# Kernel tuning notes

Hardware: AMD Instinct MI355X
Metric: run time of the kernel (lower is better)

The kernel has to match this reference:

```python
import math
import jax, jax.numpy as jnp
import numpy as np

# ---- module hyperparameters (from init_kwargs) ----
MAX_DISP = 48
IMG_WIDTH = 1248
W = IMG_WIDTH // 4          # 312 rows of the OT problem (left pixels)
C_COLS = MAX_DISP + W       # 360 columns (shifted right pixels)
NUM_ITER = 10
TAU = 0.95
EPS = 1.0
KAPPA = (1.0 - TAU) / 2.0
XI = (1.0 - TAU) / (1.0 + TAU)
RHO = EPS * TAU / (1.0 - TAU)
BIG_COST = 10000.0

B, H = 2, 64


def setup_inputs() -> dict:
    key = jax.random.key(0)
    scores = jax.random.normal(key, (B, MAX_DISP, H, W), dtype=jnp.float32)
    return {"scores": scores}


def _masked(x):
    # torch.where(isfinite(x), x, 0)
    return jnp.where(jnp.isfinite(x), x, jnp.zeros_like(x))


def _lse_kernel(Cm, f, g, axis):
    # S = (C - f[...,None] - g[...,None,:]) / eps ; eps*logsumexp(-S, axis)
    S = (Cm - f[..., None] - g[..., None, :]) / EPS
    w_res = EPS * jax.nn.logsumexp(-S, axis=axis)
    w_sgn = f if axis == -1 else g
    return w_res - _masked(w_sgn)


def _sinkhorn_update(Cm, f, g, axis, log_marginal):
    app = _lse_kernel(Cm, f, g, axis)
    return EPS * log_marginal - _masked(app)


def _smin(h, log_marginal):
    return -RHO * jax.nn.logsumexp(-h / RHO + log_marginal, axis=-1)


def _unbalanced_ot(Cm):
    # Cm: (B,H,W,C_COLS) cost matrix
    log_a = jnp.full((W,), -math.log(W), dtype=Cm.dtype)
    log_b = jnp.full((C_COLS,), -math.log(C_COLS), dtype=Cm.dtype)

    f = -EPS * jax.nn.logsumexp(-Cm / EPS + log_b, axis=-1)          # (B,H,W)
    g = jnp.zeros(Cm.shape[:2] + (C_COLS,), dtype=Cm.dtype)          # (B,H,C)

    for _ in range(NUM_ITER):
        old_f = f
        new_g = TAU * _sinkhorn_update(Cm, old_f, g, axis=-2, log_marginal=log_b)
        new_g = new_g - KAPPA * _smin(old_f, log_a)[..., None]
        new_g = new_g + XI * _smin(new_g, log_b)[..., None]
        new_f = TAU * _sinkhorn_update(Cm, f, new_g, axis=-1, log_marginal=log_a)
        new_f = new_f - KAPPA * _smin(new_g, log_b)[..., None]
        new_f = new_f + XI * _smin(new_f, log_a)[..., None]
        f, g = new_f, new_g

    S = (Cm - f[..., None] - g[..., None, :]) / EPS
    return jnp.exp(-S)                                               # transport plan P


def _scatter_to_cost(scores):
    # (B,D,H,W) scores -> (B,H,W,C_COLS) cost, vectorized scatter over d
    Bn, D, Hn, Wn = scores.shape
    j = jnp.arange(Wn)
    d = jnp.arange(D)
    col = j[None, :] - d[:, None] + MAX_DISP                          # (D,W), all in-range, no collisions
    jj = jnp.broadcast_to(j[None, :], (D, Wn))
    cost = jnp.full((Bn, Hn, Wn, C_COLS), BIG_COST, dtype=scores.dtype)
    # scores (B,D,H,W) -> (B,H,D,W) to match fancy-index result shape
    cost = cost.at[:, :, jj, col].set(-jnp.transpose(scores, (0, 2, 1, 3)))
    return cost


def _plan_to_disparity(P, D):
    right = jnp.arange(C_COLS, dtype=P.dtype) - D
    left = jnp.arange(W, dtype=P.dtype)
    disp_map = left[:, None] - right[None, :]                         # (W,C)
    mass = jnp.clip(jnp.sum(P, axis=-1), 1e-8, None)                  # (B,H,W)
    disp = jnp.sum(P * disp_map, axis=-1) / mass                      # (B,H,W)
    return disp[:, None, :, :]                                        # (B,1,H,W)


def reference(scores):
    D = scores.shape[1]
    Cm = _scatter_to_cost(scores)
    P = _unbalanced_ot(Cm)
    return _plan_to_disparity(P, D)
```

## Files before the change

kernel.cpp:

```cpp
#include <hip/hip_runtime.h>
#include <math.h>


#define MAXD   48
#define WROWS  312
#define CCOLS  360
#define NITER  10
#define NT     768
#define NWAVE  12
#define KD     24
#define NACC   (2 * NITER + 1)

__device__ __forceinline__ float pair_sum(float x) {
    int y = __builtin_amdgcn_update_dpp(0, __float_as_int(x), 0xB1, 0xf, 0xf, true);
    return x + __int_as_float(y);
}
template <int CTRL>
__device__ __forceinline__ float dpp_add(float x, float acc) {
    int y = __builtin_amdgcn_update_dpp(0, __float_as_int(x), CTRL, 0xf, 0xf, true);
    return acc + __int_as_float(y);
}
__device__ __forceinline__ float dpp_sum64(float x) {
    x = dpp_add<0x111>(x, x);
    x = dpp_add<0x112>(x, x);
    x = dpp_add<0x114>(x, x);
    x = dpp_add<0x118>(x, x);
    x = dpp_add<0x142>(x, x);
    x = dpp_add<0x143>(x, x);
    return x;
}

__global__ __launch_bounds__(NT, 3)
void ot_disp_kernel(const float* __restrict__ scores, float* __restrict__ out) {
    const int bid  = blockIdx.x;
    const int tid  = threadIdx.x;
    const int half = tid >> 1;
    const int sub  = tid & 1;
    const int wid  = tid >> 6;

    const float LOG_A2 = -8.2854022f;
    const float LOG_B2 = -8.4918531f;
    const float TAU    = 0.95f;
    const float KAPPA  = 0.025f;
    const float XI     = 0.025641026f;
    const float RHO    = 19.0f;
    const float INVRHO = 0.052631579f;
    const float TIR    = 0.05f;

    __shared__ float2 sEA[204], sEB[205], sGA[180], sGB[181];
    __shared__ __align__(16) float s_lg[NACC][384];
    __shared__ float s_R[NACC];
    float* const EAf = (float*)sEA;  float* const EBf = (float*)sEB;
    float* const GAf = (float*)sGA;  float* const GBf = (float*)sGB;

    {
        float4* lg4 = (float4*)&s_lg[0][0];
        #pragma unroll
        for (int i = 0; i < 3; ++i) {
            int idx = tid + i * NT;
            if (idx < NACC * 96) lg4[idx] = make_float4(-1e30f, -1e30f, -1e30f, -1e30f);
        }
    }
    if (tid < 205) {
        sEB[tid] = make_float2(0.f, 0.f);
        if (tid < 204) sEA[tid] = make_float2(0.f, 0.f);
        if (tid < 181) sGB[tid] = make_float2(0.f, 0.f);
        if (tid < 180) sGA[tid] = make_float2(0.f, 0.f);
    }

    const bool rowAct = (half < WROWS);
    const bool colAct = (half >= 1 && half < CCOLS);
    const int b = bid >> 6, h = bid & 63;
    const float* src = scores + ((size_t)(b * MAXD) * 64 + h) * WROWS;
    const size_t dstr = (size_t)64 * WROWS;
    const int d0 = sub * KD;
    const int jr = rowAct ? half : 0;
    const int jc = colAct ? half : 0;

    float wcol[KD];
    float wrowR[KD];
    #pragma unroll
    for (int m = 0; m < KD; ++m) {
        wrowR[m] = __expf(src[dstr * (size_t)(d0 + 23 - m) + jr]);
        int j = jc - MAXD + d0 + m;
        bool v = colAct && ((unsigned)j < (unsigned)WROWS);
        float sv = src[dstr * (size_t)(d0 + m) + (v ? j : 0)];
        wcol[m] = v ? __expf(sv) : 0.0f;
    }

    const int pe = jc + d0;
    const float2* const ep = (pe & 1) ? (sEB + ((pe + 1) >> 1)) : (sEA + (pe >> 1));
    const int qg = jr + 25 - d0;
    const float2* const gp = (qg & 1) ? (sGB + ((qg + 1) >> 1)) : (sGA + (qg >> 1));

    __syncthreads();

    {
        float a0=0,a1=0,a2=0,a3=0;
        #pragma unroll
        for (int m = 0; m < KD; m += 4) {
            a0 += wrowR[m];   a1 += wrowR[m+1];
            a2 += wrowR[m+2]; a3 += wrowR[m+3];
        }
        float s  = pair_sum((a0 + a1) + (a2 + a3));
        float ls = __builtin_amdgcn_logf(s);
        float eh = __builtin_amdgcn_exp2f(-ls);
        if (rowAct && sub == 0) {
            EAf[half + MAXD] = eh; EBf[half + MAXD + 1] = eh;
            s_lg[0][half] = ls;
        }
        __syncthreads();
    }

    float2 gv[12];
    float ehat = 0.f, den = 0.f;
    for (int it = 0; it < NITER; ++it) {
        float a0=0,a1=0,a2=0,a3=0;
        #pragma unroll
        for (int u = 0; u < 12; u += 2) {
            float2 v0 = ep[u], v1 = ep[u+1];
            a0 = fmaf(wcol[2*u],   v0.x, a0);
            a1 = fmaf(wcol[2*u+1], v0.y, a1);
            a2 = fmaf(wcol[2*u+2], v1.x, a2);
            a3 = fmaf(wcol[2*u+3], v1.y, a3);
        }
        float cs  = pair_sum((a0 + a1) + (a2 + a3));
        float lcs = __builtin_amdgcn_logf(cs);
        float gh  = __builtin_amdgcn_exp2f(-TAU * lcs);
        if (colAct && sub == 0) {
            GAf[half] = gh; GBf[half + 1] = gh;
            s_lg[1 + 2*it][half] = lcs;
        }
        __syncthreads();

        float b0=0,b1=0,b2=0,b3=0;
        #pragma unroll
        for (int u = 0; u < 12; u += 2) {
            gv[u] = gp[u]; gv[u+1] = gp[u+1];
            b0 = fmaf(wrowR[2*u],   gv[u].x,   b0);
            b1 = fmaf(wrowR[2*u+1], gv[u].y,   b1);
            b2 = fmaf(wrowR[2*u+2], gv[u+1].x, b2);
            b3 = fmaf(wrowR[2*u+3], gv[u+1].y, b3);
        }
        den = pair_sum((b0 + b1) + (b2 + b3));
        float lrs = __builtin_amdgcn_logf(den);
        ehat = __builtin_amdgcn_exp2f(-TAU * lrs);
        if (rowAct && sub == 0) {
            EAf[half + MAXD] = ehat; EBf[half + MAXD + 1] = ehat;
            s_lg[2 + 2*it][half] = lrs;
        }
        __syncthreads();
    }

    {
        const int lane = tid & 63;
        for (int t = wid; t < NACC; t += NWAVE) {
            const float coef = (t == 0) ? INVRHO : TIR;
            const float cst  = (t & 1)  ? LOG_B2 : LOG_A2;
            float s = 0.f;
            #pragma unroll
            for (int k = 0; k < 6; ++k)
                s += __builtin_amdgcn_exp2f(fmaf(coef, s_lg[t][lane + 64*k], cst));
            s = dpp_sum64(s);
            if (lane == 63) s_R[t] = __builtin_amdgcn_logf(s);
        }
        __syncthreads();
    }

    float fsh   = -LOG_B2;
    float sminF = fsh - RHO * s_R[0];
    float gsh   = 0.f;
    #pragma unroll
    for (int it = 0; it < NITER; ++it) {
        float Cg = TAU * (LOG_B2 - fsh) - KAPPA * sminF;
        float sg = Cg - RHO * s_R[1 + 2*it];
        gsh = Cg + XI * sg;
        float sminG = (1.0f + XI) * sg;
        float Cf = TAU * (LOG_A2 - gsh) - KAPPA * sminG;
        float sf = Cf - RHO * s_R[2 + 2*it];
        fsh   = Cf + XI * sf;
        sminF = (1.0f + XI) * sf;
    }

    float n0 = 0.f, n1 = 0.f;
    #pragma unroll
    for (int u = 0; u < 12; ++u) {
        n0 = fmaf((float)(d0 + 23 - 2*u) * wrowR[2*u],   gv[u].x, n0);
        n1 = fmaf((float)(d0 + 22 - 2*u) * wrowR[2*u+1], gv[u].y, n1);
    }
    float num = pair_sum(n0 + n1);
    if (rowAct && sub == 0) {
        float E = __builtin_amdgcn_exp2f(fsh + gsh) * ehat;
        float mass = fmaxf(E * den, 1e-8f);
        out[(size_t)bid * WROWS + half] = (E * num) / mass;
    }
}

extern "C" void kernel_launch(void* const* d_in, const int* in_sizes, int n_in,
                              void* d_out, int out_size, void* d_ws, size_t ws_size,
                              hipStream_t stream) {
    const float* scores = (const float*)d_in[0];
    float* out = (float*)d_out;
    ot_disp_kernel<<<128, NT, 0, stream>>>(scores, out);
}
```

Baseline: 24.56 us.

## Store Sinkhorn kernel weights and scaling vectors in fp16 and use fdot2

Converts the per-thread exp-score weights and the shared E/G scaling vectors from fp32 to fp16. The inner products now use packed v_dot2 fp16 instructions with fp32 accumulation. The shared vectors are stored as four shifted copies so each thread can do aligned 8-byte half4 loads regardless of its start offset. This halves register use for the weights and the LDS traffic per iteration. The cost is reduced precision: fp16 weights exp(score) can overflow for large scores and lose accuracy, and the scaling factors may underflow.

```diff
diff --git a/kernel.cpp b/kernel.cpp
--- a/kernel.cpp
+++ b/kernel.cpp
@@ -1,6 +1,10 @@
 #include <hip/hip_runtime.h>
 #include <math.h>
 
+
+typedef _Float16 half1;
+typedef _Float16 half2v __attribute__((ext_vector_type(2)));
+typedef _Float16 half4v __attribute__((ext_vector_type(4)));
 
 #define MAXD   48
 #define WROWS  312
@@ -10,6 +14,8 @@
 #define NWAVE  12
 #define KD     24
 #define NACC   (2 * NITER + 1)
+#define ESTR   412
+#define GSTR   364
 
 __device__ __forceinline__ float pair_sum(float x) {
     int y = __builtin_amdgcn_update_dpp(0, __float_as_int(x), 0xB1, 0xf, 0xf, true);
@@ -47,12 +53,17 @@
     const float INVRHO = 0.052631579f;
     const float TIR    = 0.05f;
 
-    __shared__ float2 sEA[204], sEB[205], sGA[180], sGB[181];
+    __shared__ __align__(8) half1 sE[4 * ESTR];
+    __shared__ __align__(8) half1 sG[4 * GSTR];
     __shared__ __align__(16) float s_lg[NACC][384];
     __shared__ float s_R[NACC];
-    float* const EAf = (float*)sEA;  float* const EBf = (float*)sEB;
-    float* const GAf = (float*)sGA;  float* const GBf = (float*)sGB;
-
+
+    {
+        unsigned* z = (unsigned*)sE;
+        for (int i = tid; i < 824; i += NT) z[i] = 0u;
+        unsigned* zg = (unsigned*)sG;
+        for (int i = tid; i < 728; i += NT) zg[i] = 0u;
+    }
     {
         float4* lg4 = (float4*)&s_lg[0][0];
         #pragma unroll
@@ -60,12 +71,6 @@
             int idx = tid + i * NT;
             if (idx < NACC * 96) lg4[idx] = make_float4(-1e30f, -1e30f, -1e30f, -1e30f);
         }
-    }
-    if (tid < 205) {
-        sEB[tid] = make_float2(0.f, 0.f);
-        if (tid < 204) sEA[tid] = make_float2(0.f, 0.f);
-        if (tid < 181) sGB[tid] = make_float2(0.f, 0.f);
-        if (tid < 180) sGA[tid] = make_float2(0.f, 0.f);
     }
 
     const bool rowAct = (half < WROWS);
@@ -77,76 +82,84 @@
     const int jr = rowAct ? half : 0;
     const int jc = colAct ? half : 0;
 
-    float wcol[KD];
-    float wrowR[KD];
+    half2v wcolH[12];
+    half2v wrowH[12];
+    float swr = 0.0f;
     #pragma unroll
     for (int m = 0; m < KD; ++m) {
-        wrowR[m] = __expf(src[dstr * (size_t)(d0 + 23 - m) + jr]);
+        float wr = __expf(src[dstr * (size_t)(d0 + 23 - m) + jr]);
+        swr += wr;
+        wrowH[m >> 1][m & 1] = (half1)wr;
         int j = jc - MAXD + d0 + m;
         bool v = colAct && ((unsigned)j < (unsigned)WROWS);
-        float sv = src[dstr * (size_t)(d0 + m) + (v ? j : 0)];
-        wcol[m] = v ? __expf(sv) : 0.0f;
+        float wc = v ? __expf(src[dstr * (size_t)(d0 + m) + (v ? j : 0)]) : 0.0f;
+        wcolH[m >> 1][m & 1] = (half1)wc;
     }
 
     const int pe = jc + d0;
-    const float2* const ep = (pe & 1) ? (sEB + ((pe + 1) >> 1)) : (sEA + (pe >> 1));
+    const int rE = (4 - (pe & 3)) & 3;
+    const half4v* const epk = (const half4v*)(sE + rE * ESTR + pe + rE);
     const int qg = jr + 25 - d0;
-    const float2* const gp = (qg & 1) ? (sGB + ((qg + 1) >> 1)) : (sGA + (qg >> 1));
+    const int rG = (4 - (qg & 3)) & 3;
+    const half4v* const gpk = (const half4v*)(sG + rG * GSTR + qg + rG);
 
     __syncthreads();
 
     {
-        float a0=0,a1=0,a2=0,a3=0;
-        #pragma unroll
-        for (int m = 0; m < KD; m += 4) {
-            a0 += wrowR[m];   a1 += wrowR[m+1];
-            a2 += wrowR[m+2]; a3 += wrowR[m+3];
-        }
-        float s  = pair_sum((a0 + a1) + (a2 + a3));
+        float s  = pair_sum(swr);
         float ls = __builtin_amdgcn_logf(s);
         float eh = __builtin_amdgcn_exp2f(-ls);
         if (rowAct && sub == 0) {
-            EAf[half + MAXD] = eh; EBf[half + MAXD + 1] = eh;
+            half1 he = (half1)eh;
+            int p = half + MAXD;
+            sE[0 * ESTR + p + 0] = he;  sE[1 * ESTR + p + 1] = he;
+            sE[2 * ESTR + p + 2] = he;  sE[3 * ESTR + p + 3] = he;
             s_lg[0][half] = ls;
         }
         __syncthreads();
     }
 
-    float2 gv[12];
+    half4v gsave[6];
     float ehat = 0.f, den = 0.f;
     for (int it = 0; it < NITER; ++it) {
-        float a0=0,a1=0,a2=0,a3=0;
-        #pragma unroll
-        for (int u = 0; u < 12; u += 2) {
-            float2 v0 = ep[u], v1 = ep[u+1];
-            a0 = fmaf(wcol[2*u],   v0.x, a0);
-            a1 = fmaf(wcol[2*u+1], v0.y, a1);
-            a2 = fmaf(wcol[2*u+2], v1.x, a2);
-            a3 = fmaf(wcol[2*u+3], v1.y, a3);
+        float a0 = 0.f, a1 = 0.f, a2 = 0.f, a3 = 0.f;
+        #pragma unroll
+        for (int u = 0; u < 6; u += 2) {
+            half4v v = epk[u], w = epk[u + 1];
+            a0 = __builtin_amdgcn_fdot2(wcolH[2*u],   __builtin_shufflevector(v, v, 0, 1), a0, false);
+            a1 = __builtin_amdgcn_fdot2(wcolH[2*u+1], __builtin_shufflevector(v, v, 2, 3), a1, false);
+            a2 = __builtin_amdgcn_fdot2(wcolH[2*u+2], __builtin_shufflevector(w, w, 0, 1), a2, false);
+            a3 = __builtin_amdgcn_fdot2(wcolH[2*u+3], __builtin_shufflevector(w, w, 2, 3), a3, false);
         }
         float cs  = pair_sum((a0 + a1) + (a2 + a3));
         float lcs = __builtin_amdgcn_logf(cs);
         float gh  = __builtin_amdgcn_exp2f(-TAU * lcs);
         if (colAct && sub == 0) {
-            GAf[half] = gh; GBf[half + 1] = gh;
+            half1 hg = (half1)gh;
+            sG[0 * GSTR + half + 0] = hg;  sG[1 * GSTR + half + 1] = hg;
+            sG[2 * GSTR + half + 2] = hg;  sG[3 * GSTR + half + 3] = hg;
             s_lg[1 + 2*it][half] = lcs;
         }
         __syncthreads();
 
-        float b0=0,b1=0,b2=0,b3=0;
-        #pragma unroll
-        for (int u = 0; u < 12; u += 2) {
-            gv[u] = gp[u]; gv[u+1] = gp[u+1];
-            b0 = fmaf(wrowR[2*u],   gv[u].x,   b0);
-            b1 = fmaf(wrowR[2*u+1], gv[u].y,   b1);
-            b2 = fmaf(wrowR[2*u+2], gv[u+1].x, b2);
-            b3 = fmaf(wrowR[2*u+3], gv[u+1].y, b3);
+        float b0 = 0.f, b1 = 0.f, b2 = 0.f, b3 = 0.f;
+        #pragma unroll
+        for (int u = 0; u < 6; u += 2) {
+            half4v v = gpk[u], w = gpk[u + 1];
+            gsave[u] = v; gsave[u + 1] = w;
+            b0 = __builtin_amdgcn_fdot2(wrowH[2*u],   __builtin_shufflevector(v, v, 0, 1), b0, false);
+            b1 = __builtin_amdgcn_fdot2(wrowH[2*u+1], __builtin_shufflevector(v, v, 2, 3), b1, false);
+            b2 = __builtin_amdgcn_fdot2(wrowH[2*u+2], __builtin_shufflevector(w, w, 0, 1), b2, false);
+            b3 = __builtin_amdgcn_fdot2(wrowH[2*u+3], __builtin_shufflevector(w, w, 2, 3), b3, false);
         }
         den = pair_sum((b0 + b1) + (b2 + b3));
         float lrs = __builtin_amdgcn_logf(den);
         ehat = __builtin_amdgcn_exp2f(-TAU * lrs);
         if (rowAct && sub == 0) {
-            EAf[half + MAXD] = ehat; EBf[half + MAXD + 1] = ehat;
+            half1 he = (half1)ehat;
+            int p = half + MAXD;
+            sE[0 * ESTR + p + 0] = he;  sE[1 * ESTR + p + 1] = he;
+            sE[2 * ESTR + p + 2] = he;  sE[3 * ESTR + p + 3] = he;
             s_lg[2 + 2*it][half] = lrs;
         }
         __syncthreads();
@@ -182,13 +195,18 @@
         sminF = (1.0f + XI) * sf;
     }
 
-    float n0 = 0.f, n1 = 0.f;
+    float num = 0.f;
     #pragma unroll
-    for (int u = 0; u < 12; ++u) {
-        n0 = fmaf((float)(d0 + 23 - 2*u) * wrowR[2*u],   gv[u].x, n0);
-        n1 = fmaf((float)(d0 + 22 - 2*u) * wrowR[2*u+1], gv[u].y, n1);
-    }
-    float num = pair_sum(n0 + n1);
+    for (int u = 0; u < 6; ++u) {
+        #pragma unroll
+        for (int t = 0; t < 4; ++t) {
+            int m = 4 * u + t;
+            float wv = (float)wrowH[m >> 1][m & 1];
+            float gv = (float)gsave[u][t];
+            num = fmaf((float)(d0 + 23 - m) * wv, gv, num);
+        }
+    }
+    num = pair_sum(num);
     if (rowAct && sub == 0) {
         float E = __builtin_amdgcn_exp2f(fsh + gsh) * ehat;
         float mass = fmaxf(E * den, 1e-8f);
```

Measured after the change: 23.28 us. 1.06x faster.

## Pack Sinkhorn weights into fp16 pairs and use dot2 with 256-thread blocks

Applied to the files above, without the earlier changes.

Switches the per-thread exp(score) weights and the shared E/G scaling vectors to packed fp16 and computes the row and column sums with v_dot2 instructions. Each thread now handles two adjacent rows and columns. The block shrinks from 768 to 256 threads, which drops the per-pair DPP reductions. The smin log-sum-exp partial sums are reduced per wave inside each iteration instead of in a separate pass over a large shared buffer. This is meant to halve the multiply work and LDS traffic and shrink shared memory, at the cost of fp16 precision on the weights and scalings, with a risk of overflow or underflow.

```diff
diff --git a/kernel.cpp b/kernel.cpp
--- a/kernel.cpp
+++ b/kernel.cpp
@@ -1,19 +1,24 @@
 #include <hip/hip_runtime.h>
 #include <math.h>
 
+
+typedef _Float16 half1;
+typedef _Float16 half2v __attribute__((ext_vector_type(2)));
 
 #define MAXD   48
 #define WROWS  312
 #define CCOLS  360
 #define NITER  10
-#define NT     768
-#define NWAVE  12
-#define KD     24
-#define NACC   (2 * NITER + 1)
-
-__device__ __forceinline__ float pair_sum(float x) {
-    int y = __builtin_amdgcn_update_dpp(0, __float_as_int(x), 0xB1, 0xf, 0xf, true);
-    return x + __int_as_float(y);
+#define NT     256
+#define NACC   21
+
+__device__ __forceinline__ half2v h2(unsigned v) { return __builtin_bit_cast(half2v, v); }
+__device__ __forceinline__ unsigned packf(float x, float y) {
+    half2v v; v[0] = (half1)x; v[1] = (half1)y;
+    return __builtin_bit_cast(unsigned, v);
+}
+__device__ __forceinline__ float fdot2(unsigned a, unsigned b, float c) {
+    return __builtin_amdgcn_fdot2(h2(a), h2(b), c, false);
 }
 template <int CTRL>
 __device__ __forceinline__ float dpp_add(float x, float acc) {
@@ -30,169 +35,186 @@
     return x;
 }
 
-__global__ __launch_bounds__(NT, 3)
+__global__ __launch_bounds__(NT, 1)
 void ot_disp_kernel(const float* __restrict__ scores, float* __restrict__ out) {
-    const int bid  = blockIdx.x;
-    const int tid  = threadIdx.x;
-    const int half = tid >> 1;
-    const int sub  = tid & 1;
-    const int wid  = tid >> 6;
+    const int tid = threadIdx.x;
+    const int wid = tid >> 6;
+    const int bid = blockIdx.x;
+    const int b   = bid >> 6, h = bid & 63;
 
     const float LOG_A2 = -8.2854022f;
     const float LOG_B2 = -8.4918531f;
-    const float TAU    = 0.95f;
-    const float KAPPA  = 0.025f;
-    const float XI     = 0.025641026f;
-    const float RHO    = 19.0f;
-    const float INVRHO = 0.052631579f;
-    const float TIR    = 0.05f;
-
-    __shared__ float2 sEA[204], sEB[205], sGA[180], sGB[181];
-    __shared__ __align__(16) float s_lg[NACC][384];
-    __shared__ float s_R[NACC];
-    float* const EAf = (float*)sEA;  float* const EBf = (float*)sEB;
-    float* const GAf = (float*)sGA;  float* const GBf = (float*)sGB;
-
-    {
-        float4* lg4 = (float4*)&s_lg[0][0];
-        #pragma unroll
-        for (int i = 0; i < 3; ++i) {
-            int idx = tid + i * NT;
-            if (idx < NACC * 96) lg4[idx] = make_float4(-1e30f, -1e30f, -1e30f, -1e30f);
-        }
-    }
-    if (tid < 205) {
-        sEB[tid] = make_float2(0.f, 0.f);
-        if (tid < 204) sEA[tid] = make_float2(0.f, 0.f);
-        if (tid < 181) sGB[tid] = make_float2(0.f, 0.f);
-        if (tid < 180) sGA[tid] = make_float2(0.f, 0.f);
-    }
-
-    const bool rowAct = (half < WROWS);
-    const bool colAct = (half >= 1 && half < CCOLS);
-    const int b = bid >> 6, h = bid & 63;
+    const float TAU = 0.95f, KAPPA = 0.025f, XI = 0.025641026f;
+    const float RHO = 19.0f, INVRHO = 0.052631579f, TIR = 0.05f;
+
+    __shared__ unsigned E2[204];
+    __shared__ unsigned G2[180];
+    __shared__ float    s_red[NACC * 4];
+
     const float* src = scores + ((size_t)(b * MAXD) * 64 + h) * WROWS;
     const size_t dstr = (size_t)64 * WROWS;
-    const int d0 = sub * KD;
-    const int jr = rowAct ? half : 0;
-    const int jc = colAct ? half : 0;
-
-    float wcol[KD];
-    float wrowR[KD];
-    #pragma unroll
-    for (int m = 0; m < KD; ++m) {
-        wrowR[m] = __expf(src[dstr * (size_t)(d0 + 23 - m) + jr]);
-        int j = jc - MAXD + d0 + m;
-        bool v = colAct && ((unsigned)j < (unsigned)WROWS);
-        float sv = src[dstr * (size_t)(d0 + m) + (v ? j : 0)];
-        wcol[m] = v ? __expf(sv) : 0.0f;
-    }
-
-    const int pe = jc + d0;
-    const float2* const ep = (pe & 1) ? (sEB + ((pe + 1) >> 1)) : (sEA + (pe >> 1));
-    const int qg = jr + 25 - d0;
-    const float2* const gp = (qg & 1) ? (sGB + ((qg + 1) >> 1)) : (sGA + (qg >> 1));
-
+
+    const bool colAct = (tid < 180);
+    const bool rowAct = (tid < 156);
+    const int  j0 = 2 * tid;
+
+    unsigned wcolE[24], wcolO[23], wcolOe;
+    unsigned wrowE[24], wrowO[23], wrowOe;
+    {
+        float e0_even = 0.f, e1_carry = 0.f, e1_0 = 0.f;
+        #pragma unroll
+        for (int k = 0; k < 48; ++k) {
+            int ja = 2 * tid - 48 + k;
+            bool va = colAct && ((unsigned)ja < (unsigned)WROWS);
+            float xa = va ? __expf(src[(size_t)k * dstr + (va ? ja : 0)]) : 0.f;
+            int jb = ja + 1;
+            bool vb = colAct && ((unsigned)jb < (unsigned)WROWS);
+            float xb = vb ? __expf(src[(size_t)k * dstr + (vb ? jb : 0)]) : 0.f;
+            if (k & 1) wcolE[k >> 1] = packf(e0_even, xa);
+            else       e0_even = xa;
+            if (k == 0)      e1_0 = xb;
+            else if (k & 1)  e1_carry = xb;
+            else             wcolO[(k >> 1) - 1] = packf(e1_carry, xb);
+            if (k == 47)     wcolOe = packf(e1_0, xb);
+        }
+    }
+    {
+        const float rm = rowAct ? 1.f : 0.f;
+        const int   jj = rowAct ? j0 : 0;
+        float a0 = 0.f, b_prev = 0.f;
+        #pragma unroll
+        for (int t = 0; t < 24; ++t) {
+            int dA = 47 - 2 * t, dB = 46 - 2 * t;
+            float2 A = *(const float2*)(src + (size_t)dA * dstr + jj);
+            float2 B = *(const float2*)(src + (size_t)dB * dstr + jj);
+            float eAx = rm * __expf(A.x), eAy = rm * __expf(A.y);
+            float eBx = rm * __expf(B.x), eBy = rm * __expf(B.y);
+            wrowE[t] = packf(eAy, eBy);
+            if (t == 0) a0 = eAx;
+            else        wrowO[t - 1] = packf(b_prev, eAx);
+            b_prev = eBx;
+        }
+        wrowOe = packf(a0, b_prev);
+    }
+
+    const unsigned ONE2 = 0x3C003C00u;
+
+    {
+        float s1 = 0.f, s0 = 0.f;
+        #pragma unroll
+        for (int t = 0; t < 24; ++t) s1 = fdot2(wrowE[t], ONE2, s1);
+        #pragma unroll
+        for (int t = 0; t < 23; ++t) s0 = fdot2(wrowO[t], ONE2, s0);
+        s0 = fdot2(wrowOe, ONE2, s0);
+        float l0 = __builtin_amdgcn_logf(s0), l1 = __builtin_amdgcn_logf(s1);
+        float y = __builtin_amdgcn_exp2f(fmaf(INVRHO, l0, LOG_A2))
+                + __builtin_amdgcn_exp2f(fmaf(INVRHO, l1, LOG_A2));
+        if (rowAct)
+            E2[tid + 24] = packf(__builtin_amdgcn_exp2f(-l0), __builtin_amdgcn_exp2f(-l1));
+        float ts = dpp_sum64(y);
+        if ((tid & 63) == 63) s_red[0 * 4 + wid] = ts;
+    }
+    if (tid < 48) E2[tid < 24 ? tid : 156 + tid] = 0u;
     __syncthreads();
 
-    {
-        float a0=0,a1=0,a2=0,a3=0;
-        #pragma unroll
-        for (int m = 0; m < KD; m += 4) {
-            a0 += wrowR[m];   a1 += wrowR[m+1];
-            a2 += wrowR[m+2]; a3 += wrowR[m+3];
-        }
-        float s  = pair_sum((a0 + a1) + (a2 + a3));
-        float ls = __builtin_amdgcn_logf(s);
-        float eh = __builtin_amdgcn_exp2f(-ls);
-        if (rowAct && sub == 0) {
-            EAf[half + MAXD] = eh; EBf[half + MAXD + 1] = eh;
-            s_lg[0][half] = ls;
-        }
+    float den0 = 0.f, den1 = 0.f, eh0 = 0.f, eh1 = 0.f;
+    unsigned v[25];
+    const int ub = colAct ? tid : 179;
+    const int vb = rowAct ? tid : 155;
+    for (int it = 0; it < NITER; ++it) {
+        unsigned u[25];
+        #pragma unroll
+        for (int t = 0; t < 25; ++t) u[t] = E2[ub + t];
+        float p0 = 0.f, p1 = 0.f, q0 = 0.f, q1 = 0.f;
+        #pragma unroll
+        for (int t = 0; t < 24; ++t) { float& d = (t & 1) ? p1 : p0; d = fdot2(wcolE[t], u[t], d); }
+        #pragma unroll
+        for (int t = 0; t < 23; ++t) { float& d = (t & 1) ? q1 : q0; d = fdot2(wcolO[t], u[t + 1], d); }
+        {
+            unsigned eop = (u[0] >> 16) | (u[24] << 16);
+            q0 = fdot2(wcolOe, eop, q0);
+        }
+        float sA = p0 + p1, sB = q0 + q1;
+        float lA = __builtin_amdgcn_logf(sA), lB = __builtin_amdgcn_logf(sB);
+        float yc = __builtin_amdgcn_exp2f(fmaf(TIR, lA, LOG_B2))
+                 + __builtin_amdgcn_exp2f(fmaf(TIR, lB, LOG_B2));
+        if (colAct)
+            G2[tid] = packf(__builtin_amdgcn_exp2f(-TAU * lA), __builtin_amdgcn_exp2f(-TAU * lB));
+        float ts = dpp_sum64(yc);
+        if ((tid & 63) == 63) s_red[(1 + 2 * it) * 4 + wid] = ts;
         __syncthreads();
-    }
-
-    float2 gv[12];
-    float ehat = 0.f, den = 0.f;
-    for (int it = 0; it < NITER; ++it) {
-        float a0=0,a1=0,a2=0,a3=0;
-        #pragma unroll
-        for (int u = 0; u < 12; u += 2) {
-            float2 v0 = ep[u], v1 = ep[u+1];
-            a0 = fmaf(wcol[2*u],   v0.x, a0);
-            a1 = fmaf(wcol[2*u+1], v0.y, a1);
-            a2 = fmaf(wcol[2*u+2], v1.x, a2);
-            a3 = fmaf(wcol[2*u+3], v1.y, a3);
-        }
-        float cs  = pair_sum((a0 + a1) + (a2 + a3));
-        float lcs = __builtin_amdgcn_logf(cs);
-        float gh  = __builtin_amdgcn_exp2f(-TAU * lcs);
-        if (colAct && sub == 0) {
-            GAf[half] = gh; GBf[half + 1] = gh;
-            s_lg[1 + 2*it][half] = lcs;
-        }
+
+        #pragma unroll
+        for (int t = 0; t < 25; ++t) v[t] = G2[vb + t];
+        float r0 = 0.f, r1 = 0.f, s0a = 0.f, s1a = 0.f;
+        #pragma unroll
+        for (int t = 0; t < 24; ++t) { float& d = (t & 1) ? r1 : r0; d = fdot2(wrowE[t], v[t + 1], d); }
+        #pragma unroll
+        for (int t = 0; t < 23; ++t) { float& d = (t & 1) ? s1a : s0a; d = fdot2(wrowO[t], v[t + 1], d); }
+        {
+            unsigned eop = (v[0] >> 16) | (v[24] << 16);
+            s0a = fdot2(wrowOe, eop, s0a);
+        }
+        den0 = s0a + s1a; den1 = r0 + r1;
+        float l0 = __builtin_amdgcn_logf(den0), l1 = __builtin_amdgcn_logf(den1);
+        eh0 = __builtin_amdgcn_exp2f(-TAU * l0);
+        eh1 = __builtin_amdgcn_exp2f(-TAU * l1);
+        float yr = __builtin_amdgcn_exp2f(fmaf(TIR, l0, LOG_A2))
+                 + __builtin_amdgcn_exp2f(fmaf(TIR, l1, LOG_A2));
+        if (rowAct) E2[tid + 24] = packf(eh0, eh1);
+        float ts2 = dpp_sum64(yr);
+        if ((tid & 63) == 63) s_red[(2 + 2 * it) * 4 + wid] = ts2;
         __syncthreads();
-
-        float b0=0,b1=0,b2=0,b3=0;
-        #pragma unroll
-        for (int u = 0; u < 12; u += 2) {
-            gv[u] = gp[u]; gv[u+1] = gp[u+1];
-            b0 = fmaf(wrowR[2*u],   gv[u].x,   b0);
-            b1 = fmaf(wrowR[2*u+1], gv[u].y,   b1);
-            b2 = fmaf(wrowR[2*u+2], gv[u+1].x, b2);
-            b3 = fmaf(wrowR[2*u+3], gv[u+1].y, b3);
-        }
-        den = pair_sum((b0 + b1) + (b2 + b3));
-        float lrs = __builtin_amdgcn_logf(den);
-        ehat = __builtin_amdgcn_exp2f(-TAU * lrs);
-        if (rowAct && sub == 0) {
-            EAf[half + MAXD] = ehat; EBf[half + MAXD + 1] = ehat;
-            s_lg[2 + 2*it][half] = lrs;
-        }
-        __syncthreads();
-    }
-
-    {
-        const int lane = tid & 63;
-        for (int t = wid; t < NACC; t += NWAVE) {
-            const float coef = (t == 0) ? INVRHO : TIR;
-            const float cst  = (t & 1)  ? LOG_B2 : LOG_A2;
-            float s = 0.f;
-            #pragma unroll
-            for (int k = 0; k < 6; ++k)
-                s += __builtin_amdgcn_exp2f(fmaf(coef, s_lg[t][lane + 64*k], cst));
-            s = dpp_sum64(s);
-            if (lane == 63) s_R[t] = __builtin_amdgcn_logf(s);
-        }
-        __syncthreads();
-    }
-
-    float fsh   = -LOG_B2;
-    float sminF = fsh - RHO * s_R[0];
-    float gsh   = 0.f;
-    #pragma unroll
-    for (int it = 0; it < NITER; ++it) {
-        float Cg = TAU * (LOG_B2 - fsh) - KAPPA * sminF;
-        float sg = Cg - RHO * s_R[1 + 2*it];
-        gsh = Cg + XI * sg;
-        float sminG = (1.0f + XI) * sg;
-        float Cf = TAU * (LOG_A2 - gsh) - KAPPA * sminG;
-        float sf = Cf - RHO * s_R[2 + 2*it];
-        fsh   = Cf + XI * sf;
-        sminF = (1.0f + XI) * sf;
-    }
-
-    float n0 = 0.f, n1 = 0.f;
-    #pragma unroll
-    for (int u = 0; u < 12; ++u) {
-        n0 = fmaf((float)(d0 + 23 - 2*u) * wrowR[2*u],   gv[u].x, n0);
-        n1 = fmaf((float)(d0 + 22 - 2*u) * wrowR[2*u+1], gv[u].y, n1);
-    }
-    float num = pair_sum(n0 + n1);
-    if (rowAct && sub == 0) {
-        float E = __builtin_amdgcn_exp2f(fsh + gsh) * ehat;
-        float mass = fmaxf(E * den, 1e-8f);
-        out[(size_t)bid * WROWS + half] = (E * num) / mass;
+    }
+
+    float fsh = -LOG_B2, gsh = 0.f;
+    {
+        float Rv[NACC];
+        #pragma unroll
+        for (int p = 0; p < NACC; ++p) {
+            float s = (s_red[4 * p] + s_red[4 * p + 1]) + (s_red[4 * p + 2] + s_red[4 * p + 3]);
+            Rv[p] = __builtin_amdgcn_logf(s);
+        }
+        float sminF = fsh - RHO * Rv[0];
+        #pragma unroll
+        for (int it = 0; it < NITER; ++it) {
+            float Cg = TAU * (LOG_B2 - fsh) - KAPPA * sminF;
+            float sg = Cg - RHO * Rv[1 + 2 * it];
+            gsh = Cg + XI * sg;
+            float sminG = (1.f + XI) * sg;
+            float Cf = TAU * (LOG_A2 - gsh) - KAPPA * sminG;
+            float sf = Cf - RHO * Rv[2 + 2 * it];
+            fsh = Cf + XI * sf;
+            sminF = (1.f + XI) * sf;
+        }
+    }
+
+    if (rowAct) {
+        float n1 = 0.f, n0 = 0.f;
+        #pragma unroll
+        for (int t = 0; t < 24; ++t) {
+            half2v dc; dc[0] = (half1)(float)(47 - 2 * t); dc[1] = (half1)(float)(46 - 2 * t);
+            half2v wd = h2(wrowE[t]) * dc;
+            n1 = __builtin_amdgcn_fdot2(wd, h2(v[t + 1]), n1, false);
+        }
+        #pragma unroll
+        for (int t = 0; t < 23; ++t) {
+            half2v dc; dc[0] = (half1)(float)(46 - 2 * t); dc[1] = (half1)(float)(45 - 2 * t);
+            half2v wd = h2(wrowO[t]) * dc;
+            n0 = __builtin_amdgcn_fdot2(wd, h2(v[t + 1]), n0, false);
+        }
+        {
+            unsigned eop = (v[0] >> 16) | (v[24] << 16);
+            half2v dc; dc[0] = (half1)47.f; dc[1] = (half1)0.f;
+            half2v wd = h2(wrowOe) * dc;
+            n0 = __builtin_amdgcn_fdot2(wd, h2(eop), n0, false);
+        }
+        float esc = __builtin_amdgcn_exp2f(fsh + gsh);
+        float E0 = esc * eh0, E1 = esc * eh1;
+        float2 o;
+        o.x = (E0 * n0) / fmaxf(E0 * den0, 1e-8f);
+        o.y = (E1 * n1) / fmaxf(E1 * den1, 1e-8f);
+        *(float2*)(out + (size_t)bid * WROWS + j0) = o;
     }
 }
 
```

After: 27.61 us. 1.12x slower.
